# Kernel optimization log

Hardware: AMD Instinct MI355X
Metric: run time of the kernel (lower is better)

## Reference

```python
import jax, jax.numpy as jnp
import numpy as np

N = 50000      # nodes
E = 800000     # edges per relation (avg degree 16)
D = 128        # in_feat == out_feat
H = 4          # num_heads
DH = D // H    # head dim = 32
NEG_SLOPE = 0.2  # DGL GATConv default


def setup_inputs() -> dict:
    key = jax.random.key(0)
    ks = jax.random.split(key, 12)
    inp = {
        "x": jax.random.normal(ks[0], (N, D), jnp.float32),
        "W_r0": jax.random.normal(ks[1], (D, D), jnp.float32) * (1.0 / np.sqrt(D)),
        "attn_l_r0": jax.random.normal(ks[2], (H, DH), jnp.float32),
        "attn_r_r0": jax.random.normal(ks[3], (H, DH), jnp.float32),
        "W_r1": jax.random.normal(ks[4], (D, D), jnp.float32) * (1.0 / np.sqrt(D)),
        "attn_l_r1": jax.random.normal(ks[5], (H, DH), jnp.float32),
        "attn_r_r1": jax.random.normal(ks[6], (H, DH), jnp.float32),
        "loop_weight": jax.random.normal(ks[7], (D, D), jnp.float32) * (1.0 / np.sqrt(D)),
        "h_bias": jnp.zeros((D,), jnp.float32),
        "src_r0": jax.random.randint(ks[8], (E,), 0, N, jnp.int32),
        "dst_r0": jax.random.randint(ks[9], (E,), 0, N, jnp.int32),
        "src_r1": jax.random.randint(ks[10], (E,), 0, N, jnp.int32),
        "dst_r1": jax.random.randint(ks[11], (E,), 0, N, jnp.int32),
    }
    return inp


def _gat_conv(x, W, attn_l, attn_r, src, dst):
    """One DGL-style GATConv (no bias, no conv activation). Returns [N,H,DH]."""
    feat = (x @ W).reshape(N, H, DH)                 # projected features
    el = jnp.einsum('nhd,hd->nh', feat, attn_l)      # [N,H] attn on source
    er = jnp.einsum('nhd,hd->nh', feat, attn_r)      # [N,H] attn on dest
    e = jax.nn.leaky_relu(el[src] + er[dst], NEG_SLOPE)  # [E,H]
    # edge softmax over incoming edges of each dst node (stable)
    emax = jax.ops.segment_max(e, dst, num_segments=N)   # [N,H]
    ex = jnp.exp(e - emax[dst])                          # [E,H]
    denom = jax.ops.segment_sum(ex, dst, num_segments=N) # [N,H]
    alpha = ex / denom[dst]                              # [E,H]
    msg = feat[src] * alpha[:, :, None]                  # [E,H,DH]
    return jax.ops.segment_sum(msg, dst, num_segments=N) # [N,H,DH]


def reference(x, W_r0, attn_l_r0, attn_r_r0, W_r1, attn_l_r1, attn_r_r1,
              loop_weight, h_bias, src_r0, dst_r0, src_r1, dst_r1):
    # HeteroGraphConv with default 'sum' cross-relation aggregation
    h = _gat_conv(x, W_r0, attn_l_r0, attn_r_r0, src_r0, dst_r0) \
      + _gat_conv(x, W_r1, attn_l_r1, attn_r_r1, src_r1, dst_r1)
    h = h.reshape(N, H * DH)          # flatten heads -> [N, out_feat]
    h = h + x @ loop_weight           # self loop
    h = h + h_bias                    # bias
    h = jax.nn.relu(h)                # activation (dropout=0, no norm, no FFN)
    return h
```

## Files before the change

### kernel.cpp

```cpp
#include <hip/hip_runtime.h>
#include <hip/hip_bf16.h>

#define NN 50000
#define EE 800000
#define DD 128
#define HH 4
#define NEG_SLOPE 0.2f

#define BSH 9
#define NBUCK 98
#define CH 8192
#define NBLK 98
#define NSEG (2 * NBUCK * NBLK)
#define BKB (2 * NBLK)
#define SORTB (2 * NBUCK)
#define ELRB 3125
#define PJB ((NN + 127) / 128)
#define WB 192

typedef __attribute__((ext_vector_type(8))) short bf16x8;
typedef __attribute__((ext_vector_type(4))) float f32x4;
typedef __attribute__((ext_vector_type(8))) unsigned short ushrt8;

static __device__ __forceinline__ float bf2f(ushort u) {
    union { unsigned int ui; float f; } v; v.ui = ((unsigned int)u) << 16; return v.f;
}
static __device__ __forceinline__ void split1(float v, ushort& h, ushort& l) {
    __hip_bfloat16 hb = __float2bfloat16(v);
    float hf = __bfloat162float(hb);
    __hip_bfloat16 lb = __float2bfloat16(v - hf);
    h = *(ushort*)&hb; l = *(ushort*)&lb;
}

__global__ __launch_bounds__(256) void prep_kernel(
    const float* __restrict__ W0, const float* __restrict__ W1,
    const float* __restrict__ Wl,
    const float* __restrict__ al0, const float* __restrict__ ar0,
    const float* __restrict__ al1, const float* __restrict__ ar1,
    const int* __restrict__ dst0, const int* __restrict__ dst1,
    ushort* __restrict__ wt, float* __restrict__ uvec, int* __restrict__ hist)
{
    const int b = blockIdx.x;
    const int t = threadIdx.x;
    if (b < WB) {
        int idx = b * 256 + t;
        int m = idx >> 14, e = idx & 16383;
        const float* W = (m == 0) ? W0 : (m == 1) ? W1 : Wl;
        int k = e >> 7, n = e & 127;
        ushort h, l; split1(W[e], h, l);
        int q = m * 4 + (k >> 5);
        int kin8 = (k >> 3) & 3, ke = k & 7;
        int sw = n & 7;
        size_t base = (size_t)q * 8192 + n * 64;
        wt[base + (((0 | kin8) ^ sw) << 3) + ke] = h;
        wt[base + (((4 | kin8) ^ sw) << 3) + ke] = l;
    } else if (b < WB + BKB) {
        __shared__ int cnt[NBUCK];
        int hb = b - WB;
        int rel = hb >= NBLK;
        int ci = hb - rel * NBLK;
        const int* __restrict__ dstA = rel ? dst1 : dst0;
        if (t < NBUCK) cnt[t] = 0;
        __syncthreads();
        int lo = ci * CH, hi = min(lo + CH, EE);
        for (int i = lo + t; i < hi; i += 256)
            atomicAdd(&cnt[dstA[i] >> BSH], 1);
        __syncthreads();
        if (t < NBUCK)
            hist[((rel * NBUCK) + t) * NBLK + ci] = cnt[t];
    } else {
        #pragma unroll
        for (int j = 0; j < 8; ++j) {
            int idx = t * 8 + j;
            int v = idx >> 7, k = idx & 127;
            int rel = v >> 3, lr = (v >> 2) & 1, h = v & 3;
            const float* W = rel ? W1 : W0;
            const float* a = rel ? (lr ? ar1 : al1) : (lr ? ar0 : al0);
            float s = 0.f;
            for (int d2 = 0; d2 < 32; ++d2)
                s += W[k * 128 + h * 32 + d2] * a[h * 32 + d2];
            uvec[v * 128 + k] = s;
        }
    }
}

__global__ __launch_bounds__(256) void scan_kernel(
    const int* __restrict__ hist, int* __restrict__ base)
{
    __shared__ int wq[4];
    const int t = threadIdx.x;
    const int lane = t & 63, wv = t >> 6;
    const int st = t * 76;
    const int en = min(st + 76, NSEG);
    int sum = 0;
    for (int i = st; i < en; ++i) sum += hist[i];
    int incl = sum;
    #pragma unroll
    for (int off = 1; off < 64; off <<= 1) {
        int u = __shfl_up(incl, off);
        if (lane >= off) incl += u;
    }
    if (lane == 63) wq[wv] = incl;
    __syncthreads();
    int woff = 0;
    #pragma unroll
    for (int w = 0; w < 4; ++w) woff += (w < wv) ? wq[w] : 0;
    int run = woff + incl - sum;
    for (int i = st; i < en; ++i) { base[i] = run; run += hist[i]; }
}

__global__ __launch_bounds__(256) void bucketelr_kernel(
    const int* __restrict__ src0, const int* __restrict__ dst0,
    const int* __restrict__ src1, const int* __restrict__ dst1,
    const int* __restrict__ base, unsigned int* __restrict__ pk,
    const float* __restrict__ x, const float* __restrict__ uvec,
    float* __restrict__ el0, float* __restrict__ er0,
    float* __restrict__ el1, float* __restrict__ er1)
{
    __shared__ float sm[2048];
    const int t = threadIdx.x;

    if (blockIdx.x < BKB) {
        int* cnt = (int*)sm;
        int* bs  = cnt + 128;
        const int hb = blockIdx.x;
        const int rel = hb >= NBLK;
        const int ci = hb - rel * NBLK;
        const int* __restrict__ srcA = rel ? src1 : src0;
        const int* __restrict__ dstA = rel ? dst1 : dst0;
        if (t < NBUCK) {
            cnt[t] = 0;
            bs[t] = base[((rel * NBUCK) + t) * NBLK + ci];
        }
        __syncthreads();
        int lo = ci * CH, hi = min(lo + CH, EE);
        for (int i = lo + t; i < hi; i += 256) {
            int dd = dstA[i], ss = srcA[i];
            int bk = dd >> BSH;
            int rk = atomicAdd(&cnt[bk], 1);
            pk[bs[bk] + rk] = (unsigned int)ss | ((unsigned int)(dd & 511) << 17);
        }
        return;
    }

    for (int i = t; i < 2048; i += 256) sm[i] = uvec[i];
    __syncthreads();
    const int lane = t & 63, wave = t >> 6;
    const int l16 = lane & 15;
    const int r = (blockIdx.x - BKB) * 16 + wave * 4 + (lane >> 4);
    float xr[8];
    if (r < NN) {
        float4 a = *(const float4*)&x[(size_t)r * DD + l16 * 8];
        float4 b2 = *(const float4*)&x[(size_t)r * DD + l16 * 8 + 4];
        xr[0] = a.x; xr[1] = a.y; xr[2] = a.z; xr[3] = a.w;
        xr[4] = b2.x; xr[5] = b2.y; xr[6] = b2.z; xr[7] = b2.w;
    } else {
        #pragma unroll
        for (int j = 0; j < 8; ++j) xr[j] = 0.f;
    }
    float s[16];
    #pragma unroll
    for (int v = 0; v < 16; ++v) {
        float acc = 0.f;
        const float* u = &sm[v * 128 + l16 * 8];
        #pragma unroll
        for (int j = 0; j < 8; ++j) acc += xr[j] * u[j];
        s[v] = acc;
    }
    #pragma unroll
    for (int m = 1; m < 16; m <<= 1)
        #pragma unroll
        for (int v = 0; v < 16; ++v) s[v] += __shfl_xor(s[v], m);
    if (r < NN) {
        float val = s[0];
        #pragma unroll
        for (int v = 1; v < 16; ++v) val = (l16 == v) ? s[v] : val;
        float* p = (l16 & 8) ? ((l16 & 4) ? er1 : el1)
                             : ((l16 & 4) ? er0 : el0);
        p[(size_t)r * 4 + (l16 & 3)] = val;
    }
}

__global__ __launch_bounds__(256) void projsort_kernel(
    const unsigned int* __restrict__ pk, const int* __restrict__ base,
    const float* __restrict__ el0, const float* __restrict__ er0,
    const float* __restrict__ el1, const float* __restrict__ er1,
    float* __restrict__ wbuf,
    int* __restrict__ row0, int* __restrict__ row1,
    int* __restrict__ list, float* __restrict__ alphaAll,
    const float* __restrict__ x, const ushort* __restrict__ wt,
    const float* __restrict__ bias,
    ushort* __restrict__ fb0, ushort* __restrict__ fb1,
    float* __restrict__ out)
{
    __shared__ ushort lds[2][8192];
    const int t = threadIdx.x;

    if (blockIdx.x < SORTB) {
        float* er_s = (float*)&lds[0][0];
        float* den  = er_s + 2048;
        int* cnt    = (int*)(den + 2048);
        int* offs   = cnt + 512;
        int* wq     = offs + 512;
        const int hb = blockIdx.x;
        const int lane = t & 63, wv = t >> 6;
        const int rel = hb >= NBUCK;
        const int bk = hb - rel * NBUCK;
        const int fs = base[((rel * NBUCK) + bk) * NBLK];
        const int fe = (rel == 1 && bk == NBUCK - 1) ? 2 * EE
                     : base[((rel * NBUCK) + bk + 1) * NBLK];
        const float* __restrict__ elA = rel ? el1 : el0;
        const float* __restrict__ erA = rel ? er1 : er0;
        const int d0 = bk << BSH;

        for (int j = t; j < 512; j += 256) {
            int d = d0 + j;
            float4 e = make_float4(0.f, 0.f, 0.f, 0.f);
            if (d < NN) e = *(const float4*)&erA[(size_t)d * 4];
            *(float4*)&er_s[j * 4] = e;
            *(float4*)&den[j * 4] = make_float4(0.f, 0.f, 0.f, 0.f);
            cnt[j] = 0;
        }
        __syncthreads();

        for (int i = fs + t; i < fe; i += 256) {
            unsigned int u = pk[i];
            int s = u & 0x1FFFF, ld = u >> 17;
            atomicAdd(&cnt[ld], 1);
            float4 e = *(const float4*)&elA[(size_t)s * 4];
            float4 rr = *(const float4*)&er_s[ld * 4];
            float4 w;
            float v;
            v = e.x + rr.x; v = v > 0.f ? v : NEG_SLOPE * v; w.x = __expf(v);
            v = e.y + rr.y; v = v > 0.f ? v : NEG_SLOPE * v; w.y = __expf(v);
            v = e.z + rr.z; v = v > 0.f ? v : NEG_SLOPE * v; w.z = __expf(v);
            v = e.w + rr.w; v = v > 0.f ? v : NEG_SLOPE * v; w.w = __expf(v);
            *(float4*)&wbuf[(size_t)i * 4] = w;
            atomicAdd(&den[ld * 4 + 0], w.x);
            atomicAdd(&den[ld * 4 + 1], w.y);
            atomicAdd(&den[ld * 4 + 2], w.z);
            atomicAdd(&den[ld * 4 + 3], w.w);
        }
        __syncthreads();

        int a = cnt[2 * t], bvl = cnt[2 * t + 1];
        int ps = a + bvl;
        int incl = ps;
        #pragma unroll
        for (int off = 1; off < 64; off <<= 1) {
            int u = __shfl_up(incl, off);
            if (lane >= off) incl += u;
        }
        if (lane == 63) wq[wv] = incl;
        __syncthreads();
        int woff = 0;
        #pragma unroll
        for (int w = 0; w < 4; ++w) woff += (w < wv) ? wq[w] : 0;
        int excl = woff + incl - ps;
        offs[2 * t] = excl;
        offs[2 * t + 1] = excl + a;
        __syncthreads();

        int* __restrict__ row = rel ? row1 : row0;
        const int fsLocal = fs - (rel ? EE : 0);
        for (int j = t; j < 512; j += 256) {
            int d = d0 + j;
            if (d < NN) row[d] = fsLocal + offs[j] + cnt[j];
        }
        for (int j = t; j < 2048; j += 256)
            den[j] = 1.f / den[j];
        __syncthreads();

        for (int i = fs + t; i < fe; i += 256) {
            unsigned int u = pk[i];
            int s = u & 0x1FFFF, ld = u >> 17;
            int p = atomicAdd(&offs[ld], 1);
            float4 w = *(const float4*)&wbuf[(size_t)i * 4];
            float4 dn = *(const float4*)&den[ld * 4];
            float4 al4 = make_float4(w.x * dn.x, w.y * dn.y, w.z * dn.z, w.w * dn.w);
            list[fs + p] = s;
            *(float4*)&alphaAll[(size_t)(fs + p) * 4] = al4;
        }
        return;
    }

    const int pb = blockIdx.x - SORTB;
    const int lane = t & 63, wave = t >> 6;
    const int l15 = lane & 15, lg = lane >> 4;
    const int rb = pb * 128 + wave * 32;

    int ra0 = rb + l15;      if (ra0 > NN - 1) ra0 = NN - 1;
    int ra1 = rb + 16 + l15; if (ra1 > NN - 1) ra1 = NN - 1;
    const int kb = lg * 8;

    bf16x8 Ah0[4], Av0[4], Ah1[4], Av1[4];
    #pragma unroll
    for (int kc = 0; kc < 4; ++kc) {
        const float* p0 = &x[(size_t)ra0 * DD + kc * 32 + kb];
        const float* p1 = &x[(size_t)ra1 * DD + kc * 32 + kb];
        float4 f0a = *(const float4*)p0, f0b = *(const float4*)(p0 + 4);
        float4 f1a = *(const float4*)p1, f1b = *(const float4*)(p1 + 4);
        float t0[8] = {f0a.x, f0a.y, f0a.z, f0a.w, f0b.x, f0b.y, f0b.z, f0b.w};
        float t1[8] = {f1a.x, f1a.y, f1a.z, f1a.w, f1b.x, f1b.y, f1b.z, f1b.w};
        union { bf16x8 v; ushort u[8]; } H0, L0, H1, L1;
        #pragma unroll
        for (int j = 0; j < 8; ++j) {
            split1(t0[j], H0.u[j], L0.u[j]);
            split1(t1[j], H1.u[j], L1.u[j]);
        }
        Ah0[kc] = H0.v; Av0[kc] = L0.v;
        Ah1[kc] = H1.v; Av1[kc] = L1.v;
    }

    {
        const bf16x8* g = (const bf16x8*)wt;
        bf16x8* L = (bf16x8*)lds[0];
        #pragma unroll
        for (int i = 0; i < 4; ++i) L[t + i * 256] = g[t + i * 256];
    }

    for (int m = 0; m < 3; ++m) {
        f32x4 acc0[8], acc1[8];
        #pragma unroll
        for (int nt = 0; nt < 8; ++nt) {
            acc0[nt] = (f32x4){0.f, 0.f, 0.f, 0.f};
            acc1[nt] = (f32x4){0.f, 0.f, 0.f, 0.f};
        }

        #pragma unroll
        for (int kc = 0; kc < 4; ++kc) {
            const int q = m * 4 + kc;
            __syncthreads();
            bf16x8 st0, st1, st2, st3;
            const bool hasNext = (q < 11);
            if (hasNext) {
                const bf16x8* g = (const bf16x8*)(wt + (size_t)(q + 1) * 8192);
                st0 = g[t]; st1 = g[t + 256]; st2 = g[t + 512]; st3 = g[t + 768];
            }
            const ushort* __restrict__ L = lds[kc & 1];
            #pragma unroll
            for (int nt = 0; nt < 8; ++nt) {
                const int n = nt * 16 + l15;
                const int sw = n & 7;
                bf16x8 bh = *(const bf16x8*)&L[n * 64 + (((0 | lg) ^ sw) << 3)];
                bf16x8 bv = *(const bf16x8*)&L[n * 64 + (((4 | lg) ^ sw) << 3)];
                acc0[nt] = __builtin_amdgcn_mfma_f32_16x16x32_bf16(Ah0[kc], bh, acc0[nt], 0, 0, 0);
                acc0[nt] = __builtin_amdgcn_mfma_f32_16x16x32_bf16(Ah0[kc], bv, acc0[nt], 0, 0, 0);
                acc0[nt] = __builtin_amdgcn_mfma_f32_16x16x32_bf16(Av0[kc], bh, acc0[nt], 0, 0, 0);
                acc1[nt] = __builtin_amdgcn_mfma_f32_16x16x32_bf16(Ah1[kc], bh, acc1[nt], 0, 0, 0);
                acc1[nt] = __builtin_amdgcn_mfma_f32_16x16x32_bf16(Ah1[kc], bv, acc1[nt], 0, 0, 0);
                acc1[nt] = __builtin_amdgcn_mfma_f32_16x16x32_bf16(Av1[kc], bh, acc1[nt], 0, 0, 0);
            }
            if (hasNext) {
                bf16x8* Lw = (bf16x8*)lds[(kc & 1) ^ 1];
                Lw[t] = st0; Lw[t + 256] = st1; Lw[t + 512] = st2; Lw[t + 768] = st3;
            }
        }

        if (m < 2) {
            ushort* __restrict__ fb = m ? fb1 : fb0;
            #pragma unroll
            for (int tt = 0; tt < 2; ++tt)
                #pragma unroll
                for (int nt = 0; nt < 8; ++nt) {
                    const int col = nt * 16 + l15;
                    #pragma unroll
                    for (int r = 0; r < 4; ++r) {
                        const int row = rb + tt * 16 + lg * 4 + r;
                        const float v = tt ? acc1[nt][r] : acc0[nt][r];
                        if (row < NN) {
                            __hip_bfloat16 hb = __float2bfloat16(v);
                            fb[(size_t)row * DD + col] = *(ushort*)&hb;
                        }
                    }
                }
        } else {
            #pragma unroll
            for (int tt = 0; tt < 2; ++tt)
                #pragma unroll
                for (int nt = 0; nt < 8; ++nt) {
                    const int col = nt * 16 + l15;
                    const float bv = bias[col];
                    #pragma unroll
                    for (int r = 0; r < 4; ++r) {
                        const int row = rb + tt * 16 + lg * 4 + r;
                        const float v = tt ? acc1[nt][r] : acc0[nt][r];
                        if (row < NN) out[(size_t)row * DD + col] = v + bv;
                    }
                }
        }
    }
}

__global__ __launch_bounds__(256) void agg_kernel(
    const int* __restrict__ row0, const int* __restrict__ list0,
    const int* __restrict__ row1, const int* __restrict__ list1,
    const float* __restrict__ alphaAll,
    const ushort* __restrict__ fb0, const ushort* __restrict__ fb1,
    float* __restrict__ out)
{
    const int d = blockIdx.x * 4 + (threadIdx.x >> 6);
    const int lane = threadIdx.x & 63;
    if (d >= NN) return;
    const int g = lane >> 4;
    const int l16 = lane & 15;
    const int c = l16 * 8;
    const int h = l16 >> 2;

    float tot[8] = {0.f, 0.f, 0.f, 0.f, 0.f, 0.f, 0.f, 0.f};

    #pragma unroll
    for (int rel = 0; rel < 2; ++rel) {
        const int* __restrict__ rowA = rel ? row1 : row0;
        const int* __restrict__ lst  = rel ? list1 : list0;
        const ushort* __restrict__ fbA = rel ? fb1 : fb0;
        const size_t ab = rel ? (size_t)EE : 0;

        const int s0 = d ? rowA[d - 1] : 0, e0 = rowA[d];
        float acc[8] = {0.f, 0.f, 0.f, 0.f, 0.f, 0.f, 0.f, 0.f};

        int i = s0 + g;
        float aA = 0.f;
        ushrt8 fA = (ushrt8){0, 0, 0, 0, 0, 0, 0, 0};
        if (i < e0) {
            int s = lst[i];
            aA = alphaAll[(ab + (size_t)i) * 4 + h];
            fA = *(const ushrt8*)&fbA[(size_t)s * DD + c];
        }
        while (i < e0) {
            const int inext = i + 4;
            float aB = 0.f;
            ushrt8 fB = (ushrt8){0, 0, 0, 0, 0, 0, 0, 0};
            if (inext < e0) {
                int s = lst[inext];
                aB = alphaAll[(ab + (size_t)inext) * 4 + h];
                fB = *(const ushrt8*)&fbA[(size_t)s * DD + c];
            }
            #pragma unroll
            for (int q = 0; q < 8; ++q) acc[q] += aA * bf2f(fA[q]);
            i = inext; aA = aB; fA = fB;
        }

        #pragma unroll
        for (int q = 0; q < 8; ++q) {
            acc[q] += __shfl_xor(acc[q], 16);
            acc[q] += __shfl_xor(acc[q], 32);
            tot[q] += acc[q];
        }
    }

    if (g == 0) {
        float4 o1 = *(float4*)&out[(size_t)d * DD + c];
        float4 o2 = *(float4*)&out[(size_t)d * DD + c + 4];
        o1.x = fmaxf(o1.x + tot[0], 0.f); o1.y = fmaxf(o1.y + tot[1], 0.f);
        o1.z = fmaxf(o1.z + tot[2], 0.f); o1.w = fmaxf(o1.w + tot[3], 0.f);
        o2.x = fmaxf(o2.x + tot[4], 0.f); o2.y = fmaxf(o2.y + tot[5], 0.f);
        o2.z = fmaxf(o2.z + tot[6], 0.f); o2.w = fmaxf(o2.w + tot[7], 0.f);
        *(float4*)&out[(size_t)d * DD + c] = o1;
        *(float4*)&out[(size_t)d * DD + c + 4] = o2;
    }
}

extern "C" void kernel_launch(void* const* d_in, const int* in_sizes, int n_in,
                              void* d_out, int out_size, void* d_ws, size_t ws_size,
                              hipStream_t stream)
{
    const float* x    = (const float*)d_in[0];
    const float* W0   = (const float*)d_in[1];
    const float* al0  = (const float*)d_in[2];
    const float* ar0  = (const float*)d_in[3];
    const float* W1   = (const float*)d_in[4];
    const float* al1  = (const float*)d_in[5];
    const float* ar1  = (const float*)d_in[6];
    const float* Wl   = (const float*)d_in[7];
    const float* bias = (const float*)d_in[8];
    const int* src0   = (const int*)d_in[9];
    const int* dst0   = (const int*)d_in[10];
    const int* src1   = (const int*)d_in[11];
    const int* dst1   = (const int*)d_in[12];
    float* out = (float*)d_out;

    float* wsf      = (float*)d_ws;
    float* wbuf     = wsf;
    float* alphaAll = wbuf + (size_t)8 * EE;
    ushort* fb0 = (ushort*)(alphaAll + (size_t)8 * EE);
    ushort* fb1 = fb0 + (size_t)NN * DD;
    ushort* wt  = fb1 + (size_t)NN * DD;
    float* uvec = (float*)(wt + 12 * 8192);
    float* el0  = uvec + 2048;
    float* er0  = el0 + (size_t)NN * HH;
    float* el1  = er0 + (size_t)NN * HH;
    float* er1  = el1 + (size_t)NN * HH;
    int* hist   = (int*)(er1 + (size_t)NN * HH);
    int* base   = hist + NSEG;
    int* row0   = base + NSEG;
    int* row1   = row0 + NN;
    unsigned int* pk = (unsigned int*)(row1 + NN);
    int* list   = (int*)(pk + (size_t)2 * EE);
    int* list0  = list;
    int* list1  = list + EE;

    prep_kernel<<<dim3(WB + BKB + 1), dim3(256), 0, stream>>>(
        W0, W1, Wl, al0, ar0, al1, ar1, dst0, dst1, wt, uvec, hist);

    scan_kernel<<<dim3(1), dim3(256), 0, stream>>>(hist, base);

    bucketelr_kernel<<<dim3(BKB + ELRB), dim3(256), 0, stream>>>(
        src0, dst0, src1, dst1, base, pk, x, uvec, el0, er0, el1, er1);

    projsort_kernel<<<dim3(SORTB + PJB), dim3(256), 0, stream>>>(
        pk, base, el0, er0, el1, er1, wbuf, row0, row1, list, alphaAll,
        x, wt, bias, fb0, fb1, out);

    agg_kernel<<<dim3((NN + 3) / 4), dim3(256), 0, stream>>>(
        row0, list0, row1, list1, alphaAll, fb0, fb1, out);
}
```

Before: 236.4 us.

## Compute edge softmax inside aggregation and split sort from projection kernel

The sort phase now only builds CSR rows and source lists. It no longer computes exp weights, denominators and normalized alphas, so the wbuf and alphaAll edge arrays and their global traffic go away. The aggregation kernel recomputes leaky-relu/exp per edge from el[src] and er[dst], accumulates an unnormalized sum plus denominator, and divides at the end. The projection and sort are now separate launches, which adds a kernel launch and loses the concurrency of the previously fused blocks. Dropping the max subtraction relies on exp not overflowing, as the old code already did.

Result: faster. 194.1 us (median of 2 runs) (-17.9%).

```diff
diff --git a/kernel.cpp b/kernel.cpp
--- a/kernel.cpp
+++ b/kernel.cpp
@@ -181,13 +181,7 @@
     }
 }
 
-__global__ __launch_bounds__(256) void projsort_kernel(
-    const unsigned int* __restrict__ pk, const int* __restrict__ base,
-    const float* __restrict__ el0, const float* __restrict__ er0,
-    const float* __restrict__ el1, const float* __restrict__ er1,
-    float* __restrict__ wbuf,
-    int* __restrict__ row0, int* __restrict__ row1,
-    int* __restrict__ list, float* __restrict__ alphaAll,
+__global__ __launch_bounds__(256) void proj_kernel(
     const float* __restrict__ x, const ushort* __restrict__ wt,
     const float* __restrict__ bias,
     ushort* __restrict__ fb0, ushort* __restrict__ fb1,
@@ -195,99 +189,9 @@
 {
     __shared__ ushort lds[2][8192];
     const int t = threadIdx.x;
-
-    if (blockIdx.x < SORTB) {
-        float* er_s = (float*)&lds[0][0];
-        float* den  = er_s + 2048;
-        int* cnt    = (int*)(den + 2048);
-        int* offs   = cnt + 512;
-        int* wq     = offs + 512;
-        const int hb = blockIdx.x;
-        const int lane = t & 63, wv = t >> 6;
-        const int rel = hb >= NBUCK;
-        const int bk = hb - rel * NBUCK;
-        const int fs = base[((rel * NBUCK) + bk) * NBLK];
-        const int fe = (rel == 1 && bk == NBUCK - 1) ? 2 * EE
-                     : base[((rel * NBUCK) + bk + 1) * NBLK];
-        const float* __restrict__ elA = rel ? el1 : el0;
-        const float* __restrict__ erA = rel ? er1 : er0;
-        const int d0 = bk << BSH;
-
-        for (int j = t; j < 512; j += 256) {
-            int d = d0 + j;
-            float4 e = make_float4(0.f, 0.f, 0.f, 0.f);
-            if (d < NN) e = *(const float4*)&erA[(size_t)d * 4];
-            *(float4*)&er_s[j * 4] = e;
-            *(float4*)&den[j * 4] = make_float4(0.f, 0.f, 0.f, 0.f);
-            cnt[j] = 0;
-        }
-        __syncthreads();
-
-        for (int i = fs + t; i < fe; i += 256) {
-            unsigned int u = pk[i];
-            int s = u & 0x1FFFF, ld = u >> 17;
-            atomicAdd(&cnt[ld], 1);
-            float4 e = *(const float4*)&elA[(size_t)s * 4];
-            float4 rr = *(const float4*)&er_s[ld * 4];
-            float4 w;
-            float v;
-            v = e.x + rr.x; v = v > 0.f ? v : NEG_SLOPE * v; w.x = __expf(v);
-            v = e.y + rr.y; v = v > 0.f ? v : NEG_SLOPE * v; w.y = __expf(v);
-            v = e.z + rr.z; v = v > 0.f ? v : NEG_SLOPE * v; w.z = __expf(v);
-            v = e.w + rr.w; v = v > 0.f ? v : NEG_SLOPE * v; w.w = __expf(v);
-            *(float4*)&wbuf[(size_t)i * 4] = w;
-            atomicAdd(&den[ld * 4 + 0], w.x);
-            atomicAdd(&den[ld * 4 + 1], w.y);
-            atomicAdd(&den[ld * 4 + 2], w.z);
-            atomicAdd(&den[ld * 4 + 3], w.w);
-        }
-        __syncthreads();
-
-        int a = cnt[2 * t], bvl = cnt[2 * t + 1];
-        int ps = a + bvl;
-        int incl = ps;
-        #pragma unroll
-        for (int off = 1; off < 64; off <<= 1) {
-            int u = __shfl_up(incl, off);
-            if (lane >= off) incl += u;
-        }
-        if (lane == 63) wq[wv] = incl;
-        __syncthreads();
-        int woff = 0;
-        #pragma unroll
-        for (int w = 0; w < 4; ++w) woff += (w < wv) ? wq[w] : 0;
-        int excl = woff + incl - ps;
-        offs[2 * t] = excl;
-        offs[2 * t + 1] = excl + a;
-        __syncthreads();
-
-        int* __restrict__ row = rel ? row1 : row0;
-        const int fsLocal = fs - (rel ? EE : 0);
-        for (int j = t; j < 512; j += 256) {
-            int d = d0 + j;
-            if (d < NN) row[d] = fsLocal + offs[j] + cnt[j];
-        }
-        for (int j = t; j < 2048; j += 256)
-            den[j] = 1.f / den[j];
-        __syncthreads();
-
-        for (int i = fs + t; i < fe; i += 256) {
-            unsigned int u = pk[i];
-            int s = u & 0x1FFFF, ld = u >> 17;
-            int p = atomicAdd(&offs[ld], 1);
-            float4 w = *(const float4*)&wbuf[(size_t)i * 4];
-            float4 dn = *(const float4*)&den[ld * 4];
-            float4 al4 = make_float4(w.x * dn.x, w.y * dn.y, w.z * dn.z, w.w * dn.w);
-            list[fs + p] = s;
-            *(float4*)&alphaAll[(size_t)(fs + p) * 4] = al4;
-        }
-        return;
-    }
-
-    const int pb = blockIdx.x - SORTB;
     const int lane = t & 63, wave = t >> 6;
     const int l15 = lane & 15, lg = lane >> 4;
-    const int rb = pb * 128 + wave * 32;
+    const int rb = blockIdx.x * 128 + wave * 32;
 
     int ra0 = rb + l15;      if (ra0 > NN - 1) ra0 = NN - 1;
     int ra1 = rb + 16 + l15; if (ra1 > NN - 1) ra1 = NN - 1;
@@ -392,10 +296,69 @@
     }
 }
 
+__global__ __launch_bounds__(256) void sort_kernel(
+    const unsigned int* __restrict__ pk, const int* __restrict__ base,
+    int* __restrict__ row0, int* __restrict__ row1, int* __restrict__ list)
+{
+    __shared__ int cnt[512];
+    __shared__ int offs[512];
+    __shared__ int wq[4];
+    const int hb = blockIdx.x;
+    const int t = threadIdx.x;
+    const int lane = t & 63, wv = t >> 6;
+    const int rel = hb >= NBUCK;
+    const int bk = hb - rel * NBUCK;
+
+    const int fs = base[((rel * NBUCK) + bk) * NBLK];
+    const int fe = (rel == 1 && bk == NBUCK - 1) ? 2 * EE
+                 : base[((rel * NBUCK) + bk + 1) * NBLK];
+
+    cnt[t] = 0; cnt[t + 256] = 0;
+    __syncthreads();
+    for (int i = fs + t; i < fe; i += 256)
+        atomicAdd(&cnt[pk[i] >> 17], 1);
+    __syncthreads();
+
+    int a = cnt[2 * t], bvl = cnt[2 * t + 1];
+    int ps = a + bvl;
+    int incl = ps;
+    #pragma unroll
+    for (int off = 1; off < 64; off <<= 1) {
+        int u = __shfl_up(incl, off);
+        if (lane >= off) incl += u;
+    }
+    if (lane == 63) wq[wv] = incl;
+    __syncthreads();
+    int woff = 0;
+    #pragma unroll
+    for (int w = 0; w < 4; ++w) woff += (w < wv) ? wq[w] : 0;
+    int excl = woff + incl - ps;
+    offs[2 * t] = excl;
+    offs[2 * t + 1] = excl + a;
+    __syncthreads();
+
+    int* __restrict__ row = rel ? row1 : row0;
+    const int fsLocal = fs - (rel ? EE : 0);
+    const int d0 = bk << BSH;
+    for (int j = t; j < 512; j += 256) {
+        int d = d0 + j;
+        if (d < NN) row[d] = fsLocal + offs[j] + cnt[j];
+    }
+    __syncthreads();
+
+    for (int i = fs + t; i < fe; i += 256) {
+        unsigned int u = pk[i];
+        int ld = u >> 17;
+        int p = atomicAdd(&offs[ld], 1);
+        list[fs + p] = (int)(u & 0x1FFFF);
+    }
+}
+
 __global__ __launch_bounds__(256) void agg_kernel(
     const int* __restrict__ row0, const int* __restrict__ list0,
+    const float* __restrict__ el0, const float* __restrict__ er0,
     const int* __restrict__ row1, const int* __restrict__ list1,
-    const float* __restrict__ alphaAll,
+    const float* __restrict__ el1, const float* __restrict__ er1,
     const ushort* __restrict__ fb0, const ushort* __restrict__ fb1,
     float* __restrict__ out)
 {
@@ -413,39 +376,51 @@
     for (int rel = 0; rel < 2; ++rel) {
         const int* __restrict__ rowA = rel ? row1 : row0;
         const int* __restrict__ lst  = rel ? list1 : list0;
+        const float* __restrict__ elA = rel ? el1 : el0;
+        const float* __restrict__ erA = rel ? er1 : er0;
         const ushort* __restrict__ fbA = rel ? fb1 : fb0;
-        const size_t ab = rel ? (size_t)EE : 0;
 
         const int s0 = d ? rowA[d - 1] : 0, e0 = rowA[d];
+        const float erh = erA[(size_t)d * 4 + h];
         float acc[8] = {0.f, 0.f, 0.f, 0.f, 0.f, 0.f, 0.f, 0.f};
+        float den = 0.f;
 
         int i = s0 + g;
-        float aA = 0.f;
+        float elvA = 0.f;
         ushrt8 fA = (ushrt8){0, 0, 0, 0, 0, 0, 0, 0};
         if (i < e0) {
             int s = lst[i];
-            aA = alphaAll[(ab + (size_t)i) * 4 + h];
+            elvA = elA[(size_t)s * 4 + h];
             fA = *(const ushrt8*)&fbA[(size_t)s * DD + c];
         }
         while (i < e0) {
             const int inext = i + 4;
-            float aB = 0.f;
+            float elvB = 0.f;
             ushrt8 fB = (ushrt8){0, 0, 0, 0, 0, 0, 0, 0};
             if (inext < e0) {
                 int s = lst[inext];
-                aB = alphaAll[(ab + (size_t)inext) * 4 + h];
+                elvB = elA[(size_t)s * 4 + h];
                 fB = *(const ushrt8*)&fbA[(size_t)s * DD + c];
             }
+            float ev = elvA + erh;
+            ev = ev > 0.f ? ev : NEG_SLOPE * ev;
+            float w = __expf(ev);
+            den += w;
             #pragma unroll
-            for (int q = 0; q < 8; ++q) acc[q] += aA * bf2f(fA[q]);
-            i = inext; aA = aB; fA = fB;
-        }
-
+            for (int q = 0; q < 8; ++q) acc[q] += w * bf2f(fA[q]);
+            i = inext; elvA = elvB; fA = fB;
+        }
+
+        den += __shfl_xor(den, 16); den += __shfl_xor(den, 32);
         #pragma unroll
         for (int q = 0; q < 8; ++q) {
             acc[q] += __shfl_xor(acc[q], 16);
             acc[q] += __shfl_xor(acc[q], 32);
-            tot[q] += acc[q];
+        }
+        if (e0 > s0) {
+            float inv = 1.f / den;
+            #pragma unroll
+            for (int q = 0; q < 8; ++q) tot[q] += acc[q] * inv;
         }
     }
 
@@ -480,10 +455,8 @@
     const int* dst1   = (const int*)d_in[12];
     float* out = (float*)d_out;
 
-    float* wsf      = (float*)d_ws;
-    float* wbuf     = wsf;
-    float* alphaAll = wbuf + (size_t)8 * EE;
-    ushort* fb0 = (ushort*)(alphaAll + (size_t)8 * EE);
+    ushort* wsu = (ushort*)d_ws;
+    ushort* fb0 = wsu;
     ushort* fb1 = fb0 + (size_t)NN * DD;
     ushort* wt  = fb1 + (size_t)NN * DD;
     float* uvec = (float*)(wt + 12 * 8192);
@@ -508,10 +481,12 @@
     bucketelr_kernel<<<dim3(BKB + ELRB), dim3(256), 0, stream>>>(
         src0, dst0, src1, dst1, base, pk, x, uvec, el0, er0, el1, er1);
 
-    projsort_kernel<<<dim3(SORTB + PJB), dim3(256), 0, stream>>>(
-        pk, base, el0, er0, el1, er1, wbuf, row0, row1, list, alphaAll,
+    proj_kernel<<<dim3(PJB), dim3(256), 0, stream>>>(
         x, wt, bias, fb0, fb1, out);
 
+    sort_kernel<<<dim3(SORTB), dim3(256), 0, stream>>>(
+        pk, base, row0, row1, list);
+
     agg_kernel<<<dim3((NN + 3) / 4), dim3(256), 0, stream>>>(
-        row0, list0, row1, list1, alphaAll, fb0, fb1, out);
-}
+        row0, list0, el0, er0, row1, list1, el1, er1, fb0, fb1, out);
+}
```
